# Performance work log

Hardware: AMD Instinct MI355X
Metric: run time of the kernel (lower is better)

Reference implementation:

```python
import jax, jax.numpy as jnp
import numpy as np

B, T, H, C, R = 8, 8192, 128, 128, 128  # batch, points, hidden, c_dim, plane reso
EPS = 1e-3  # 10e-4 in original
PLANE_COLS = ((0, 2), (0, 1), (1, 2))  # xz, xy, yz


def _normalize_coordinate(p, cols):
    # normalize_coordinate with padding=0.0: p in [-0.5,0.5] -> [0,1), clipped
    xy = p[..., jnp.array(cols)] / (1.0 + 0.0 + EPS) + 0.5
    return jnp.clip(xy, 0.0, 1.0 - EPS)


def _coordinate2index(xy):
    g = jnp.floor(xy * R).astype(jnp.int32)  # [B,T,2]
    return g[..., 0] + R * g[..., 1]  # [B,T]


def _resblock(x, w0, b0, w1, b1, ws):
    # ResnetBlockFC: fc_1(relu(fc_0(relu(x)))) + shortcut(x)
    net = jax.nn.relu(x) @ w0 + b0
    dx = jax.nn.relu(net) @ w1 + b1
    return x @ ws + dx


def _pool_local(c, idx_list):
    # c: [B,T,F]; scatter_max into R*R bins per plane, gather back, sum over planes
    def one(cb, ib):  # cb [T,F], ib [T]
        out = jnp.full((R * R, cb.shape[-1]), -jnp.inf, cb.dtype).at[ib].max(cb)
        out = jnp.where(jnp.isinf(out), jnp.zeros_like(out), out)  # empty bins -> 0
        return out[ib]  # gather-broadcast back to points
    pooled = jnp.zeros_like(c)
    for idx in idx_list:
        pooled = pooled + jax.vmap(one)(c, idx)
    return pooled


def _plane_features(cfeat, idx):
    # scatter_mean of [B,T,C] into [B, C, R, R]
    def one(cb, ib):  # cb [T,C], ib [T]
        sums = jnp.zeros((R * R, cb.shape[-1]), cb.dtype).at[ib].add(cb)
        cnt = jnp.zeros((R * R,), cb.dtype).at[ib].add(1.0)
        return sums / jnp.clip(cnt, 1.0, None)[:, None]
    m = jax.vmap(one)(cfeat, idx)  # [B, R*R, C]
    return m.transpose(0, 2, 1).reshape(cfeat.shape[0], cfeat.shape[-1], R, R)


def _forward(p, p2, wp, bp, wp2, bp2,
             blk_w0, blk_b0, blk_w1, blk_b1, blk_ws,
             blkc_w0, blkc_b0, blkc_w1, blkc_b1, blkc_ws,
             fc_c_w, fc_c_b, fc_cc_w, fc_cc_b):
    idx_list = [_coordinate2index(_normalize_coordinate(p, cols)) for cols in PLANE_COLS]

    # feat_pos (PointNetPlusPlusAttnFusion) surrogate: per-point projections + additive fusion
    net = p @ wp + bp                  # [B,T,2H] geometry stream
    net_corr = net + (p2 @ wp2 + bp2)  # [B,T,2H] fused articulation stream

    net = _resblock(net, blk_w0[0], blk_b0[0], blk_w1[0], blk_b1[0], blk_ws[0])
    for i in range(1, blk_w0.shape[0]):
        pooled = _pool_local(net, idx_list)
        net = _resblock(jnp.concatenate([net, pooled], axis=-1),
                        blk_w0[i], blk_b0[i], blk_w1[i], blk_b1[i], blk_ws[i])
    c = net @ fc_c_w + fc_c_b  # [B,T,C]

    net_corr = _resblock(net_corr, blkc_w0[0], blkc_b0[0], blkc_w1[0], blkc_b1[0], blkc_ws[0])
    for i in range(1, blkc_w0.shape[0]):
        pooled = _pool_local(net_corr, idx_list)
        net_corr = _resblock(jnp.concatenate([net_corr, pooled], axis=-1),
                             blkc_w0[i], blkc_b0[i], blkc_w1[i], blkc_b1[i], blkc_ws[i])
    c_corr = net_corr @ fc_cc_w + fc_cc_b  # [B,T,C]

    planes = [_plane_features(c, idx) for idx in idx_list]
    planes += [_plane_features(c_corr, idx) for idx in idx_list]
    # order: geo_xz, geo_xy, geo_yz, corr_xz, corr_xy, corr_yz
    return jnp.stack(planes)  # [6, B, C, R, R]


def setup_inputs() -> dict:
    key = jax.random.key(0)
    ks = jax.random.split(key, 24)
    s = 0.05
    def n(i, shape):
        return jax.random.normal(ks[i], shape, jnp.float32) * s
    NB = 5
    return {
        "p": jax.random.uniform(ks[0], (B, T, 3), jnp.float32, -0.5, 0.5),
        "p2": jax.random.uniform(ks[1], (B, T, 3), jnp.float32, -0.5, 0.5),
        "wp": n(2, (3, 2 * H)), "bp": jnp.zeros((2 * H,), jnp.float32),
        "wp2": n(3, (3, 2 * H)), "bp2": jnp.zeros((2 * H,), jnp.float32),
        "blk_w0": n(4, (NB, 2 * H, H)), "blk_b0": jnp.zeros((NB, H), jnp.float32),
        "blk_w1": n(5, (NB, H, H)), "blk_b1": jnp.zeros((NB, H), jnp.float32),
        "blk_ws": n(6, (NB, 2 * H, H)),
        "blkc_w0": n(7, (NB, 2 * H, H)), "blkc_b0": jnp.zeros((NB, H), jnp.float32),
        "blkc_w1": n(8, (NB, H, H)), "blkc_b1": jnp.zeros((NB, H), jnp.float32),
        "blkc_ws": n(9, (NB, 2 * H, H)),
        "fc_c_w": n(10, (H, C)), "fc_c_b": jnp.zeros((C,), jnp.float32),
        "fc_cc_w": n(11, (H, C)), "fc_cc_b": jnp.zeros((C,), jnp.float32),
    }


def reference(p, p2, wp, bp, wp2, bp2,
              blk_w0, blk_b0, blk_w1, blk_b1, blk_ws,
              blkc_w0, blkc_b0, blkc_w1, blkc_b1, blkc_ws,
              fc_c_w, fc_c_b, fc_cc_w, fc_cc_b):
    return _forward(p, p2, wp, bp, wp2, bp2,
                    blk_w0, blk_b0, blk_w1, blk_b1, blk_ws,
                    blkc_w0, blkc_b0, blkc_w1, blkc_b1, blkc_ws,
                    fc_c_w, fc_c_b, fc_cc_w, fc_cc_b)
```

## Files before the change

kernel.cpp:

```cpp
#include <hip/hip_runtime.h>
#include <cstdint>
#include <cstddef>

#define Bn 8
#define Tn 8192
#define BT (Bn*Tn)
#define Hn 128
#define RRn 16384

typedef unsigned short u16;
typedef __attribute__((ext_vector_type(8))) short s8v;
typedef __attribute__((ext_vector_type(4))) float f4v;

#define SSTR ((size_t)BT*128)

__device__ __forceinline__ u16 f2bf(float f) {
  unsigned u = __float_as_uint(f);
  unsigned r = (u + 0x7FFF + ((u >> 16) & 1)) >> 16;
  return (u16)r;
}
__device__ __forceinline__ unsigned pack2(float a, float b) {
  return (unsigned)f2bf(a) | ((unsigned)f2bf(b) << 16);
}

__device__ __forceinline__ s8v relu8(s8v a) {
  union { s8v s; unsigned u[4]; } x; x.s = a;
#pragma unroll
  for (int k = 0; k < 4; ++k) {
    unsigned m = ((x.u[k] & 0x80008000u) >> 15) * 0xFFFFu;
    x.u[k] &= ~m;
  }
  return x.s;
}

__device__ __forceinline__ void upk(unsigned u, float& lo, float& hi) {
  lo = __uint_as_float(u << 16);
  hi = __uint_as_float(u & 0xFFFF0000u);
}

__global__ void k_idx(const float* __restrict__ p, int* __restrict__ idx) {
  int i = blockIdx.x*256 + threadIdx.x;
  if (i >= BT) return;
  float v0 = p[i*3+0], v1 = p[i*3+1], v2 = p[i*3+2];
  float v[3] = {v0, v1, v2};
  const int A0[3] = {0,0,1};
  const int A1[3] = {2,1,2};
#pragma unroll
  for (int pl = 0; pl < 3; ++pl) {
    float a = v[A0[pl]] / 1.001f + 0.5f;
    float b = v[A1[pl]] / 1.001f + 0.5f;
    a = fminf(fmaxf(a, 0.0f), 0.999f);
    b = fminf(fmaxf(b, 0.0f), 0.999f);
    int ga = (int)floorf(a * 128.0f);
    int gb = (int)floorf(b * 128.0f);
    idx[pl*BT + i] = ga + 128*gb;
  }
}

__global__ void k_hist(const int* __restrict__ idx, int* __restrict__ cnt32) {
  int g = blockIdx.x*256 + threadIdx.x;
  if (g >= 3*BT) return;
  int pl = g >> 16, i = g & (BT-1);
  int b = i >> 13;
  atomicAdd(&cnt32[(pl*Bn + b)*RRn + idx[g]], 1);
}

__global__ void k_scan(const int* __restrict__ cnt32, int* __restrict__ starts,
                       int* __restrict__ cursor) {
  int seg = blockIdx.x;
  const int* c = cnt32 + seg*RRn;
  int* st = starts + seg*RRn;
  int* cu = cursor + seg*RRn;
  int t = threadIdx.x;
  __shared__ int part[256];
  int base = t*64;
  int sum = 0;
#pragma unroll 8
  for (int j = 0; j < 64; ++j) sum += c[base+j];
  part[t] = sum; __syncthreads();
  for (int ofs = 1; ofs < 256; ofs <<= 1) {
    int v = (t >= ofs) ? part[t-ofs] : 0;
    __syncthreads();
    part[t] += v;
    __syncthreads();
  }
  int run = (t ? part[t-1] : 0) + seg*Tn;
#pragma unroll 8
  for (int j = 0; j < 64; ++j) { st[base+j] = run; cu[base+j] = run; run += c[base+j]; }
}

__global__ void k_fill(const int* __restrict__ idx, int* __restrict__ cursor,
                       int* __restrict__ sorted) {
  int g = blockIdx.x*256 + threadIdx.x;
  if (g >= 3*BT) return;
  int pl = g >> 16, i = g & (BT-1);
  int b = i >> 13;
  int pos = atomicAdd(&cursor[(pl*Bn + b)*RRn + idx[g]], 1);
  sorted[pos] = i;
}

__global__ void k_prep(const float* __restrict__ bw0, const float* __restrict__ bw1,
                       const float* __restrict__ bws, const float* __restrict__ cw0,
                       const float* __restrict__ cw1, const float* __restrict__ cws,
                       const float* __restrict__ fcw, const float* __restrict__ fccw,
                       u16* __restrict__ arena) {
  int c = blockIdx.x;
  int s = c / 26, r = c % 26;
  const float* base;
  if (r < 10)      base = (s ? cw0 : bw0) + (size_t)(r >> 1)*32768 + (size_t)(r & 1)*16384;
  else if (r < 15) base = (s ? cw1 : bw1) + (size_t)(r - 10)*16384;
  else if (r < 25) base = (s ? cws : bws) + (size_t)((r - 15) >> 1)*32768 + (size_t)((r - 15) & 1)*16384;
  else             base = s ? fccw : fcw;
  __shared__ u16 ld[128*130];
#pragma unroll 4
  for (int it = 0; it < 64; ++it) {
    int lin = it*256 + threadIdx.x;
    int k = lin >> 7, n = lin & 127;
    ld[k*130 + n] = f2bf(base[lin]);
  }
  __syncthreads();
  u16* dst = arena + (size_t)c*16384;
#pragma unroll 4
  for (int it = 0; it < 64; ++it) {
    int lin = it*256 + threadIdx.x;
    int n = lin >> 7, k = lin & 127;
    dst[lin] = ld[k*130 + n];
  }
}

template<int MODE>
__global__ __launch_bounds__(512) void k_rb(
    const u16* __restrict__ xAb, const u16* __restrict__ xBb,
    const float* __restrict__ p, const float* __restrict__ p2,
    const float* __restrict__ wp, const float* __restrict__ bp,
    const float* __restrict__ wp2, const float* __restrict__ bp2,
    const u16* __restrict__ arena,
    int cw00, int cw01, int cws0, int cws1, int cw1c, int cfcw,
    const float* __restrict__ b0g, const float* __restrict__ b0c,
    const float* __restrict__ b1g, const float* __restrict__ b1c,
    const float* __restrict__ fcbg, const float* __restrict__ fcbc,
    u16* __restrict__ outb)
{
  const int y = blockIdx.y;
  const u16* ar = arena + (size_t)y*26*16384;
  const u16* w00 = ar + (size_t)cw00*16384;
  const u16* w01 = ar + (size_t)cw01*16384;
  const u16* ws0 = ar + (size_t)cws0*16384;
  const u16* ws1 = ar + (size_t)cws1*16384;
  const u16* w1c = ar + (size_t)cw1c*16384;
  const u16* fcw = ar + (size_t)cfcw*16384;
  const float* b0 = y ? b0c : b0g;
  const float* b1 = y ? b1c : b1g;
  const float* fcb = y ? fcbc : fcbg;
  const u16* xA = xAb + (size_t)y*SSTR;
  const u16* xB = xBb + (size_t)y*SSTR;
  u16* outp = outb + (size_t)y*SSTR;

  __shared__ u16 xs [128*72];
  __shared__ u16 w0s[128*72];
  __shared__ u16 wss[128*72];
  __shared__ u16 hid[128*136];
  const int tid = threadIdx.x;
  const size_t row0 = (size_t)blockIdx.x * 128;
  const int l = tid & 63, w = tid >> 6;
  const int lm = l & 15, lg = l >> 4;
  const int trow = tid >> 2, tq = tid & 3;

  f4v acc_h[8], acc_s[8];
#pragma unroll
  for (int j = 0; j < 8; ++j) { acc_h[j] = (f4v){0,0,0,0}; acc_s[j] = (f4v){0,0,0,0}; }

  float pa0=0.f, pa1=0.f, pa2=0.f, pq0=0.f, pq1=0.f, pq2=0.f;
  if (MODE == 1) {
    int rr = (int)row0 + trow;
    pa0 = p[rr*3+0]; pa1 = p[rr*3+1]; pa2 = p[rr*3+2];
    if (y) { pq0 = p2[rr*3+0]; pq1 = p2[rr*3+1]; pq2 = p2[rr*3+2]; }
  }

  const u16* pa  = xs  + (w*16 + lm)*72 + lg*8;
  const u16* pbh = w0s + lm*72 + lg*8;
  const u16* pbs = wss + lm*72 + lg*8;

#pragma unroll 1
  for (int kc = 0; kc < 4; ++kc) {
    const u16* xsrc  = (kc < 2) ? xA  : xB;
    const u16* w0src = (kc < 2) ? w00 : w01;
    const u16* wssrc = (kc < 2) ? ws0 : ws1;
    const int k0 = (kc & 1) * 64;
    __syncthreads();
    {
      if (MODE == 1) {
        const int c0 = (kc >> 1)*128 + k0 + tq*16;
        unsigned tmp[8];
#pragma unroll
        for (int q = 0; q < 4; ++q) {
          float4 w0v = *(const float4*)(wp + c0 + q*4);
          float4 w1v = *(const float4*)(wp + 256 + c0 + q*4);
          float4 w2v = *(const float4*)(wp + 512 + c0 + q*4);
          float4 bbv = *(const float4*)(bp + c0 + q*4);
          float v0 = pa0*w0v.x + pa1*w1v.x + pa2*w2v.x + bbv.x;
          float v1 = pa0*w0v.y + pa1*w1v.y + pa2*w2v.y + bbv.y;
          float v2 = pa0*w0v.z + pa1*w1v.z + pa2*w2v.z + bbv.z;
          float v3 = pa0*w0v.w + pa1*w1v.w + pa2*w2v.w + bbv.w;
          if (y) {
            float4 u0 = *(const float4*)(wp2 + c0 + q*4);
            float4 u1 = *(const float4*)(wp2 + 256 + c0 + q*4);
            float4 u2 = *(const float4*)(wp2 + 512 + c0 + q*4);
            float4 b2 = *(const float4*)(bp2 + c0 + q*4);
            v0 += pq0*u0.x + pq1*u1.x + pq2*u2.x + b2.x;
            v1 += pq0*u0.y + pq1*u1.y + pq2*u2.y + b2.y;
            v2 += pq0*u0.z + pq1*u1.z + pq2*u2.z + b2.z;
            v3 += pq0*u0.w + pq1*u1.w + pq2*u2.w + b2.w;
          }
          tmp[q*2]   = pack2(v0, v1);
          tmp[q*2+1] = pack2(v2, v3);
        }
        uint4* d1 = (uint4*)(xs + trow*72 + tq*16);
        d1[0] = make_uint4(tmp[0], tmp[1], tmp[2], tmp[3]);
        d1[1] = make_uint4(tmp[4], tmp[5], tmp[6], tmp[7]);
      } else {
        const u16* s1 = xsrc + (row0 + trow)*128 + k0 + tq*16;
        uint4* d1 = (uint4*)(xs + trow*72 + tq*16);
        d1[0] = ((const uint4*)s1)[0]; d1[1] = ((const uint4*)s1)[1];
      }
      const u16* s2 = w0src + trow*128 + k0 + tq*16;
      uint4* d2 = (uint4*)(w0s + trow*72 + tq*16);
      d2[0] = ((const uint4*)s2)[0]; d2[1] = ((const uint4*)s2)[1];
      const u16* s3 = wssrc + trow*128 + k0 + tq*16;
      uint4* d3 = (uint4*)(wss + trow*72 + tq*16);
      d3[0] = ((const uint4*)s3)[0]; d3[1] = ((const uint4*)s3)[1];
    }
    __syncthreads();
#pragma unroll
    for (int kk = 0; kk < 2; ++kk) {
      s8v a  = *(const s8v*)(pa + kk*32);
      s8v ar2 = relu8(a);
#pragma unroll
      for (int nj = 0; nj < 8; ++nj) {
        s8v bh = *(const s8v*)(pbh + nj*16*72 + kk*32);
        acc_h[nj] = __builtin_amdgcn_mfma_f32_16x16x32_bf16(ar2, bh, acc_h[nj], 0, 0, 0);
      }
#pragma unroll
      for (int nj = 0; nj < 8; ++nj) {
        s8v bs = *(const s8v*)(pbs + nj*16*72 + kk*32);
        acc_s[nj] = __builtin_amdgcn_mfma_f32_16x16x32_bf16(a, bs, acc_s[nj], 0, 0, 0);
      }
    }
  }
  __syncthreads();
  {
    const u16* s1 = w1c + trow*128 + tq*16;
    uint4* d1 = (uint4*)(w0s + trow*72 + tq*16);
    d1[0] = ((const uint4*)s1)[0]; d1[1] = ((const uint4*)s1)[1];
    const u16* s2 = w1c + trow*128 + 64 + tq*16;
    uint4* d2 = (uint4*)(wss + trow*72 + tq*16);
    d2[0] = ((const uint4*)s2)[0]; d2[1] = ((const uint4*)s2)[1];
#pragma unroll
    for (int nj = 0; nj < 8; ++nj) {
      const int col = nj*16 + lm;
      const float bv = b0[col];
#pragma unroll
      for (int r = 0; r < 4; ++r) {
        int row = w*16 + lg*4 + r;
        hid[row*136 + col] = f2bf(fmaxf(acc_h[nj][r] + bv, 0.0f));
      }
    }
  }
  __syncthreads();
  {
    const u16* pah = hid + (w*16 + lm)*136 + lg*8;
#pragma unroll
    for (int kk = 0; kk < 4; ++kk) {
      s8v a = *(const s8v*)(pah + kk*32);
      const u16* pb = ((kk < 2) ? w0s : wss) + lm*72 + lg*8 + (kk & 1)*32;
#pragma unroll
      for (int nj = 0; nj < 8; ++nj) {
        s8v bb = *(const s8v*)(pb + nj*16*72);
        acc_s[nj] = __builtin_amdgcn_mfma_f32_16x16x32_bf16(a, bb, acc_s[nj], 0, 0, 0);
      }
    }
  }
  if (MODE != 2) {
#pragma unroll
    for (int nj = 0; nj < 8; ++nj) {
      const int col = nj*16 + lm;
      const float bv = b1[col];
#pragma unroll
      for (int r = 0; r < 4; ++r) {
        int row = w*16 + lg*4 + r;
        outp[(row0 + row)*128 + col] = f2bf(acc_s[nj][r] + bv);
      }
    }
  } else {
    __syncthreads();
#pragma unroll
    for (int nj = 0; nj < 8; ++nj) {
      const int col = nj*16 + lm;
      const float bv = b1[col];
#pragma unroll
      for (int r = 0; r < 4; ++r) {
        int row = w*16 + lg*4 + r;
        hid[row*136 + col] = f2bf(acc_s[nj][r] + bv);
      }
    }
    const u16* s1 = fcw + trow*128 + tq*16;
    uint4* d1 = (uint4*)(w0s + trow*72 + tq*16);
    d1[0] = ((const uint4*)s1)[0]; d1[1] = ((const uint4*)s1)[1];
    const u16* s2 = fcw + trow*128 + 64 + tq*16;
    uint4* d2 = (uint4*)(wss + trow*72 + tq*16);
    d2[0] = ((const uint4*)s2)[0]; d2[1] = ((const uint4*)s2)[1];
    __syncthreads();
    f4v accf[8];
#pragma unroll
    for (int j = 0; j < 8; ++j) accf[j] = (f4v){0,0,0,0};
    const u16* pah = hid + (w*16 + lm)*136 + lg*8;
#pragma unroll
    for (int kk = 0; kk < 4; ++kk) {
      s8v a = *(const s8v*)(pah + kk*32);
      const u16* pb = ((kk < 2) ? w0s : wss) + lm*72 + lg*8 + (kk & 1)*32;
#pragma unroll
      for (int nj = 0; nj < 8; ++nj) {
        s8v bb = *(const s8v*)(pb + nj*16*72);
        accf[nj] = __builtin_amdgcn_mfma_f32_16x16x32_bf16(a, bb, accf[nj], 0, 0, 0);
      }
    }
#pragma unroll
    for (int nj = 0; nj < 8; ++nj) {
      const int col = nj*16 + lm;
      const float bv = fcb[col];
#pragma unroll
      for (int r = 0; r < 4; ++r) {
        int row = w*16 + lg*4 + r;
        outp[(row0 + row)*128 + col] = f2bf(accf[nj][r] + bv);
      }
    }
  }
}

__global__ void k_pool(const int* __restrict__ idx, const int* __restrict__ starts,
                       const int* __restrict__ cnt32, const int* __restrict__ sorted,
                       const u16* __restrict__ netb, u16* __restrict__ pooledb) {
  const u16* net = netb + (size_t)blockIdx.y*SSTR;
  u16* pooled = pooledb + (size_t)blockIdx.y*SSTR;
  int g = blockIdx.x*256 + threadIdx.x;
  int sl = g & 15;
  int i = g >> 4;
  if (i >= BT) return;
  int b = i >> 13;
  float acc[8];
#pragma unroll
  for (int k = 0; k < 8; ++k) acc[k] = 0.0f;
#pragma unroll
  for (int pl = 0; pl < 3; ++pl) {
    int seg = (pl*Bn + b)*RRn + idx[pl*BT + i];
    int s = starts[seg];
    int e = s + cnt32[seg];
    float mx[8];
#pragma unroll
    for (int k = 0; k < 8; ++k) mx[k] = -3.0e38f;
    for (int j = s; j < e; ++j) {
      int jj = sorted[j];
      uint4 v = *(const uint4*)(net + (size_t)jj*128 + sl*8);
      float lo, hi;
      upk(v.x, lo, hi); mx[0] = fmaxf(mx[0], lo); mx[1] = fmaxf(mx[1], hi);
      upk(v.y, lo, hi); mx[2] = fmaxf(mx[2], lo); mx[3] = fmaxf(mx[3], hi);
      upk(v.z, lo, hi); mx[4] = fmaxf(mx[4], lo); mx[5] = fmaxf(mx[5], hi);
      upk(v.w, lo, hi); mx[6] = fmaxf(mx[6], lo); mx[7] = fmaxf(mx[7], hi);
    }
#pragma unroll
    for (int k = 0; k < 8; ++k) acc[k] += mx[k];
  }
  union { uint4 v; unsigned u[4]; } o;
#pragma unroll
  for (int k = 0; k < 4; ++k)
    o.u[k] = (unsigned)f2bf(acc[2*k]) | ((unsigned)f2bf(acc[2*k+1]) << 16);
  *(uint4*)(pooled + (size_t)i*128 + sl*8) = o.v;
}

__global__ __launch_bounds__(256) void k_mean(
    const int* __restrict__ starts, const int* __restrict__ cnt32,
    const int* __restrict__ sorted, const u16* __restrict__ cbufb,
    float* __restrict__ out) {
  int W = blockIdx.x*4 + (threadIdx.x >> 6);
  int lane = threadIdx.x & 63;
  int grp = W & 255;
  int b = (W >> 8) & 7;
  int plq = W >> 11;
  int ss = plq / 3, pl = plq - 3*ss;
  int bin = grp*64 + lane;
  int seg = (pl*Bn + b)*RRn + bin;
  int c = cnt32[seg];
  int s0 = starts[seg];
  float inv = (c > 0) ? 1.0f/(float)c : 0.0f;
  const u16* cb = cbufb + (size_t)ss*SSTR;
  size_t obase = ((size_t)(plq*Bn + b)*Hn)*RRn + bin;
#pragma unroll 1
  for (int half = 0; half < 2; ++half) {
    float sum[64];
#pragma unroll
    for (int k = 0; k < 64; ++k) sum[k] = 0.f;
    for (int j = 0; j < c; ++j) {
      int jj = sorted[s0 + j];
      const uint4* r = (const uint4*)(cb + (size_t)jj*128 + half*64);
#pragma unroll
      for (int k = 0; k < 8; ++k) {
        uint4 q = r[k];
        float lo, hi;
        upk(q.x, lo, hi); sum[k*8+0] += lo; sum[k*8+1] += hi;
        upk(q.y, lo, hi); sum[k*8+2] += lo; sum[k*8+3] += hi;
        upk(q.z, lo, hi); sum[k*8+4] += lo; sum[k*8+5] += hi;
        upk(q.w, lo, hi); sum[k*8+6] += lo; sum[k*8+7] += hi;
      }
    }
#pragma unroll
    for (int k = 0; k < 64; ++k)
      out[obase + (size_t)(half*64 + k)*RRn] = sum[k]*inv;
  }
}

extern "C" void kernel_launch(void* const* d_in, const int* in_sizes, int n_in,
                              void* d_out_v, int out_size, void* d_ws, size_t ws_size,
                              hipStream_t stream) {
  const float* p    = (const float*)d_in[0];
  const float* p2   = (const float*)d_in[1];
  const float* wp   = (const float*)d_in[2];
  const float* bp   = (const float*)d_in[3];
  const float* wp2  = (const float*)d_in[4];
  const float* bp2  = (const float*)d_in[5];
  const float* bw0  = (const float*)d_in[6];
  const float* bb0  = (const float*)d_in[7];
  const float* bw1  = (const float*)d_in[8];
  const float* bb1  = (const float*)d_in[9];
  const float* bws  = (const float*)d_in[10];
  const float* cw0  = (const float*)d_in[11];
  const float* cb0  = (const float*)d_in[12];
  const float* cw1  = (const float*)d_in[13];
  const float* cb1  = (const float*)d_in[14];
  const float* cws  = (const float*)d_in[15];
  const float* fcw  = (const float*)d_in[16];
  const float* fcb  = (const float*)d_in[17];
  const float* fccw = (const float*)d_in[18];
  const float* fccb = (const float*)d_in[19];
  float* out = (float*)d_out_v;

  size_t off = 0;
  auto alloc = [&](size_t bytes) -> char* {
    char* r = (char*)d_ws + off;
    off += (bytes + 255) & ~(size_t)255;
    return r;
  };
  int* idx    = (int*)alloc((size_t)3*BT*4);
  int* cnt32  = (int*)alloc((size_t)3*Bn*RRn*4);
  int* starts = (int*)alloc((size_t)3*Bn*RRn*4);
  int* cursor = (int*)alloc((size_t)3*Bn*RRn*4);
  int* sorted = (int*)alloc((size_t)3*BT*4);
  u16* arena  = (u16*)alloc((size_t)52*16384*2);
  u16* buf0   = (u16*)alloc(2*SSTR*2);
  u16* buf1   = (u16*)alloc(2*SSTR*2);
  u16* bufP   = (u16*)alloc(2*SSTR*2);
  u16* cbuf   = (u16*)alloc(2*SSTR*2);
  if (off > ws_size) return;

  hipMemsetAsync(cnt32, 0, (size_t)3*Bn*RRn*4, stream);
  k_prep<<<52, 256, 0, stream>>>(bw0, bw1, bws, cw0, cw1, cws, fcw, fccw, arena);
  k_idx <<<BT/256, 256, 0, stream>>>(p, idx);
  k_hist<<<(3*BT)/256, 256, 0, stream>>>(idx, cnt32);
  k_scan<<<24, 256, 0, stream>>>(cnt32, starts, cursor);
  k_fill<<<(3*BT)/256, 256, 0, stream>>>(idx, cursor, sorted);

  k_rb<1><<<dim3(BT/128, 2), 512, 0, stream>>>(
      nullptr, nullptr, p, p2, wp, bp, wp2, bp2,
      arena, 0, 1, 15, 16, 10, 25,
      bb0, cb0, bb1, cb1, nullptr, nullptr, buf1);
  u16* net = buf1; u16* other = buf0;
  for (int blk = 1; blk < 4; ++blk) {
    k_pool<<<dim3((BT*16)/256, 2), 256, 0, stream>>>(idx, starts, cnt32, sorted, net, bufP);
    k_rb<0><<<dim3(BT/128, 2), 512, 0, stream>>>(
        net, bufP, nullptr, nullptr, nullptr, nullptr, nullptr, nullptr,
        arena, 2*blk, 2*blk+1, 15+2*blk, 16+2*blk, 10+blk, 25,
        bb0 + blk*128, cb0 + blk*128, bb1 + blk*128, cb1 + blk*128,
        nullptr, nullptr, other);
    u16* t = net; net = other; other = t;
  }
  k_pool<<<dim3((BT*16)/256, 2), 256, 0, stream>>>(idx, starts, cnt32, sorted, net, bufP);
  k_rb<2><<<dim3(BT/128, 2), 512, 0, stream>>>(
      net, bufP, nullptr, nullptr, nullptr, nullptr, nullptr, nullptr,
      arena, 8, 9, 23, 24, 14, 25,
      bb0 + 4*128, cb0 + 4*128, bb1 + 4*128, cb1 + 4*128, fcb, fccb, cbuf);

  k_mean<<<3072, 256, 0, stream>>>(starts, cnt32, sorted, cbuf, out);
}
```

Before: 609.1 us.

## Fuse local max-pooling into resblock GEMM loads and histogram into index kernel

Removes the separate k_pool kernel. Each k_rb block now computes the scatter-max pooled features for its rows on the fly while staging the second half of the K dimension into shared memory, which avoids writing and re-reading the pooled buffer. Separately, the histogram atomics move into k_idx, which drops one launch. The cost is that the irregular gather loop now sits inside the GEMM kernel's load phase, which may add register pressure and serialize behind the per-bin loops with uneven counts.

```diff
diff --git a/kernel.cpp b/kernel.cpp
--- a/kernel.cpp
+++ b/kernel.cpp
@@ -38,9 +38,11 @@
   hi = __uint_as_float(u & 0xFFFF0000u);
 }
 
-__global__ void k_idx(const float* __restrict__ p, int* __restrict__ idx) {
+__global__ void k_idx(const float* __restrict__ p, int* __restrict__ idx,
+                      int* __restrict__ cnt32) {
   int i = blockIdx.x*256 + threadIdx.x;
   if (i >= BT) return;
+  int b = i >> 13;
   float v0 = p[i*3+0], v1 = p[i*3+1], v2 = p[i*3+2];
   float v[3] = {v0, v1, v2};
   const int A0[3] = {0,0,1};
@@ -48,21 +50,15 @@
 #pragma unroll
   for (int pl = 0; pl < 3; ++pl) {
     float a = v[A0[pl]] / 1.001f + 0.5f;
-    float b = v[A1[pl]] / 1.001f + 0.5f;
+    float bq = v[A1[pl]] / 1.001f + 0.5f;
     a = fminf(fmaxf(a, 0.0f), 0.999f);
-    b = fminf(fmaxf(b, 0.0f), 0.999f);
+    bq = fminf(fmaxf(bq, 0.0f), 0.999f);
     int ga = (int)floorf(a * 128.0f);
-    int gb = (int)floorf(b * 128.0f);
-    idx[pl*BT + i] = ga + 128*gb;
-  }
-}
-
-__global__ void k_hist(const int* __restrict__ idx, int* __restrict__ cnt32) {
-  int g = blockIdx.x*256 + threadIdx.x;
-  if (g >= 3*BT) return;
-  int pl = g >> 16, i = g & (BT-1);
-  int b = i >> 13;
-  atomicAdd(&cnt32[(pl*Bn + b)*RRn + idx[g]], 1);
+    int gb = (int)floorf(bq * 128.0f);
+    int bin = ga + 128*gb;
+    idx[pl*BT + i] = bin;
+    atomicAdd(&cnt32[(pl*Bn + b)*RRn + bin], 1);
+  }
 }
 
 __global__ void k_scan(const int* __restrict__ cnt32, int* __restrict__ starts,
@@ -130,10 +126,12 @@
 
 template<int MODE>
 __global__ __launch_bounds__(512) void k_rb(
-    const u16* __restrict__ xAb, const u16* __restrict__ xBb,
+    const u16* __restrict__ xAb,
     const float* __restrict__ p, const float* __restrict__ p2,
     const float* __restrict__ wp, const float* __restrict__ bp,
     const float* __restrict__ wp2, const float* __restrict__ bp2,
+    const int* __restrict__ idxg, const int* __restrict__ startsg,
+    const int* __restrict__ cnt32g, const int* __restrict__ sortedg,
     const u16* __restrict__ arena,
     int cw00, int cw01, int cws0, int cws1, int cw1c, int cfcw,
     const float* __restrict__ b0g, const float* __restrict__ b0c,
@@ -153,7 +151,6 @@
   const float* b1 = y ? b1c : b1g;
   const float* fcb = y ? fcbc : fcbg;
   const u16* xA = xAb + (size_t)y*SSTR;
-  const u16* xB = xBb + (size_t)y*SSTR;
   u16* outp = outb + (size_t)y*SSTR;
 
   __shared__ u16 xs [128*72];
@@ -176,6 +173,15 @@
     pa0 = p[rr*3+0]; pa1 = p[rr*3+1]; pa2 = p[rr*3+2];
     if (y) { pq0 = p2[rr*3+0]; pq1 = p2[rr*3+1]; pq2 = p2[rr*3+2]; }
   }
+  int pseg0=0, psegc0=0, pseg1=0, psegc1=0, pseg2=0, psegc2=0;
+  if (MODE != 1) {
+    const int gi = (int)row0 + trow;
+    const int bb = gi >> 13;
+    int s_, c_;
+    s_ = (0*Bn + bb)*RRn + idxg[0*BT + gi]; pseg0 = startsg[s_]; psegc0 = cnt32g[s_];
+    c_ = (1*Bn + bb)*RRn + idxg[1*BT + gi]; pseg1 = startsg[c_]; psegc1 = cnt32g[c_];
+    s_ = (2*Bn + bb)*RRn + idxg[2*BT + gi]; pseg2 = startsg[s_]; psegc2 = cnt32g[s_];
+  }
 
   const u16* pa  = xs  + (w*16 + lm)*72 + lg*8;
   const u16* pbh = w0s + lm*72 + lg*8;
@@ -183,7 +189,6 @@
 
 #pragma unroll 1
   for (int kc = 0; kc < 4; ++kc) {
-    const u16* xsrc  = (kc < 2) ? xA  : xB;
     const u16* w0src = (kc < 2) ? w00 : w01;
     const u16* wssrc = (kc < 2) ? ws0 : ws1;
     const int k0 = (kc & 1) * 64;
@@ -218,10 +223,47 @@
         uint4* d1 = (uint4*)(xs + trow*72 + tq*16);
         d1[0] = make_uint4(tmp[0], tmp[1], tmp[2], tmp[3]);
         d1[1] = make_uint4(tmp[4], tmp[5], tmp[6], tmp[7]);
-      } else {
-        const u16* s1 = xsrc + (row0 + trow)*128 + k0 + tq*16;
+      } else if (kc < 2) {
+        const u16* s1 = xA + (row0 + trow)*128 + k0 + tq*16;
         uint4* d1 = (uint4*)(xs + trow*72 + tq*16);
         d1[0] = ((const uint4*)s1)[0]; d1[1] = ((const uint4*)s1)[1];
+      } else {
+        const int ch0 = k0 + tq*16;
+        float acc[16];
+#pragma unroll
+        for (int k = 0; k < 16; ++k) acc[k] = 0.f;
+        int segS[3] = {pseg0, pseg1, pseg2};
+        int segC[3] = {psegc0, psegc1, psegc2};
+#pragma unroll
+        for (int pl = 0; pl < 3; ++pl) {
+          int s0 = segS[pl];
+          int c  = segC[pl];
+          float mx[16];
+#pragma unroll
+          for (int k = 0; k < 16; ++k) mx[k] = -3.0e38f;
+          for (int j = 0; j < c; ++j) {
+            int jj = sortedg[s0 + j];
+            const uint4* r = (const uint4*)(xA + (size_t)jj*128 + ch0);
+            uint4 q0 = r[0], q1 = r[1];
+            float lo, hi;
+            upk(q0.x, lo, hi); mx[0]=fmaxf(mx[0],lo);  mx[1]=fmaxf(mx[1],hi);
+            upk(q0.y, lo, hi); mx[2]=fmaxf(mx[2],lo);  mx[3]=fmaxf(mx[3],hi);
+            upk(q0.z, lo, hi); mx[4]=fmaxf(mx[4],lo);  mx[5]=fmaxf(mx[5],hi);
+            upk(q0.w, lo, hi); mx[6]=fmaxf(mx[6],lo);  mx[7]=fmaxf(mx[7],hi);
+            upk(q1.x, lo, hi); mx[8]=fmaxf(mx[8],lo);  mx[9]=fmaxf(mx[9],hi);
+            upk(q1.y, lo, hi); mx[10]=fmaxf(mx[10],lo); mx[11]=fmaxf(mx[11],hi);
+            upk(q1.z, lo, hi); mx[12]=fmaxf(mx[12],lo); mx[13]=fmaxf(mx[13],hi);
+            upk(q1.w, lo, hi); mx[14]=fmaxf(mx[14],lo); mx[15]=fmaxf(mx[15],hi);
+          }
+#pragma unroll
+          for (int k = 0; k < 16; ++k) acc[k] += mx[k];
+        }
+        unsigned tmp[8];
+#pragma unroll
+        for (int k = 0; k < 8; ++k) tmp[k] = pack2(acc[2*k], acc[2*k+1]);
+        uint4* d1 = (uint4*)(xs + trow*72 + tq*16);
+        d1[0] = make_uint4(tmp[0], tmp[1], tmp[2], tmp[3]);
+        d1[1] = make_uint4(tmp[4], tmp[5], tmp[6], tmp[7]);
       }
       const u16* s2 = w0src + trow*128 + k0 + tq*16;
       uint4* d2 = (uint4*)(w0s + trow*72 + tq*16);
@@ -335,46 +377,6 @@
       }
     }
   }
-}
-
-__global__ void k_pool(const int* __restrict__ idx, const int* __restrict__ starts,
-                       const int* __restrict__ cnt32, const int* __restrict__ sorted,
-                       const u16* __restrict__ netb, u16* __restrict__ pooledb) {
-  const u16* net = netb + (size_t)blockIdx.y*SSTR;
-  u16* pooled = pooledb + (size_t)blockIdx.y*SSTR;
-  int g = blockIdx.x*256 + threadIdx.x;
-  int sl = g & 15;
-  int i = g >> 4;
-  if (i >= BT) return;
-  int b = i >> 13;
-  float acc[8];
-#pragma unroll
-  for (int k = 0; k < 8; ++k) acc[k] = 0.0f;
-#pragma unroll
-  for (int pl = 0; pl < 3; ++pl) {
-    int seg = (pl*Bn + b)*RRn + idx[pl*BT + i];
-    int s = starts[seg];
-    int e = s + cnt32[seg];
-    float mx[8];
-#pragma unroll
-    for (int k = 0; k < 8; ++k) mx[k] = -3.0e38f;
-    for (int j = s; j < e; ++j) {
-      int jj = sorted[j];
-      uint4 v = *(const uint4*)(net + (size_t)jj*128 + sl*8);
-      float lo, hi;
-      upk(v.x, lo, hi); mx[0] = fmaxf(mx[0], lo); mx[1] = fmaxf(mx[1], hi);
-      upk(v.y, lo, hi); mx[2] = fmaxf(mx[2], lo); mx[3] = fmaxf(mx[3], hi);
-      upk(v.z, lo, hi); mx[4] = fmaxf(mx[4], lo); mx[5] = fmaxf(mx[5], hi);
-      upk(v.w, lo, hi); mx[6] = fmaxf(mx[6], lo); mx[7] = fmaxf(mx[7], hi);
-    }
-#pragma unroll
-    for (int k = 0; k < 8; ++k) acc[k] += mx[k];
-  }
-  union { uint4 v; unsigned u[4]; } o;
-#pragma unroll
-  for (int k = 0; k < 4; ++k)
-    o.u[k] = (unsigned)f2bf(acc[2*k]) | ((unsigned)f2bf(acc[2*k+1]) << 16);
-  *(uint4*)(pooled + (size_t)i*128 + sl*8) = o.v;
 }
 
 __global__ __launch_bounds__(256) void k_mean(
@@ -457,34 +459,33 @@
   u16* arena  = (u16*)alloc((size_t)52*16384*2);
   u16* buf0   = (u16*)alloc(2*SSTR*2);
   u16* buf1   = (u16*)alloc(2*SSTR*2);
-  u16* bufP   = (u16*)alloc(2*SSTR*2);
   u16* cbuf   = (u16*)alloc(2*SSTR*2);
   if (off > ws_size) return;
 
   hipMemsetAsync(cnt32, 0, (size_t)3*Bn*RRn*4, stream);
   k_prep<<<52, 256, 0, stream>>>(bw0, bw1, bws, cw0, cw1, cws, fcw, fccw, arena);
-  k_idx <<<BT/256, 256, 0, stream>>>(p, idx);
-  k_hist<<<(3*BT)/256, 256, 0, stream>>>(idx, cnt32);
+  k_idx <<<BT/256, 256, 0, stream>>>(p, idx, cnt32);
   k_scan<<<24, 256, 0, stream>>>(cnt32, starts, cursor);
   k_fill<<<(3*BT)/256, 256, 0, stream>>>(idx, cursor, sorted);
 
   k_rb<1><<<dim3(BT/128, 2), 512, 0, stream>>>(
-      nullptr, nullptr, p, p2, wp, bp, wp2, bp2,
+      nullptr, p, p2, wp, bp, wp2, bp2,
+      nullptr, nullptr, nullptr, nullptr,
       arena, 0, 1, 15, 16, 10, 25,
       bb0, cb0, bb1, cb1, nullptr, nullptr, buf1);
   u16* net = buf1; u16* other = buf0;
   for (int blk = 1; blk < 4; ++blk) {
-    k_pool<<<dim3((BT*16)/256, 2), 256, 0, stream>>>(idx, starts, cnt32, sorted, net, bufP);
     k_rb<0><<<dim3(BT/128, 2), 512, 0, stream>>>(
-        net, bufP, nullptr, nullptr, nullptr, nullptr, nullptr, nullptr,
+        net, nullptr, nullptr, nullptr, nullptr, nullptr, nullptr,
+        idx, starts, cnt32, sorted,
         arena, 2*blk, 2*blk+1, 15+2*blk, 16+2*blk, 10+blk, 25,
         bb0 + blk*128, cb0 + blk*128, bb1 + blk*128, cb1 + blk*128,
         nullptr, nullptr, other);
     u16* t = net; net = other; other = t;
   }
-  k_pool<<<dim3((BT*16)/256, 2), 256, 0, stream>>>(idx, starts, cnt32, sorted, net, bufP);
   k_rb<2><<<dim3(BT/128, 2), 512, 0, stream>>>(
-      net, bufP, nullptr, nullptr, nullptr, nullptr, nullptr, nullptr,
+      net, nullptr, nullptr, nullptr, nullptr, nullptr, nullptr,
+      idx, starts, cnt32, sorted,
       arena, 8, 9, 23, 24, 14, 25,
       bb0 + 4*128, cb0 + 4*128, bb1 + 4*128, cb1 + 4*128, fcb, fccb, cbuf);
 
```

Result: slower. 657.0 us (+7.9%).

## Double rows per k_rb block, prefetch next K-chunk into registers, fuse histogram into k_idx

Applied to the files above, without the earlier changes.

The resblock GEMM kernel now handles 256 rows per block instead of 128. Each wave computes two 16-row MFMA tiles that share every weight fragment read from LDS. The next K-chunk of activations and weights is loaded into registers while the current chunk's MFMAs run, so global latency overlaps compute. The histogram atomics move into the index kernel, which removes one launch and one pass over idx. The cost is roughly double the accumulator registers and more LDS per block, plus half as many blocks (256 per y), which could hurt occupancy or SM fill.

```diff
diff --git a/kernel.cpp b/kernel.cpp
--- a/kernel.cpp
+++ b/kernel.cpp
@@ -38,9 +38,11 @@
   hi = __uint_as_float(u & 0xFFFF0000u);
 }
 
-__global__ void k_idx(const float* __restrict__ p, int* __restrict__ idx) {
+__global__ void k_idx(const float* __restrict__ p, int* __restrict__ idx,
+                      int* __restrict__ cnt32) {
   int i = blockIdx.x*256 + threadIdx.x;
   if (i >= BT) return;
+  int b = i >> 13;
   float v0 = p[i*3+0], v1 = p[i*3+1], v2 = p[i*3+2];
   float v[3] = {v0, v1, v2};
   const int A0[3] = {0,0,1};
@@ -48,21 +50,15 @@
 #pragma unroll
   for (int pl = 0; pl < 3; ++pl) {
     float a = v[A0[pl]] / 1.001f + 0.5f;
-    float b = v[A1[pl]] / 1.001f + 0.5f;
+    float bq = v[A1[pl]] / 1.001f + 0.5f;
     a = fminf(fmaxf(a, 0.0f), 0.999f);
-    b = fminf(fmaxf(b, 0.0f), 0.999f);
+    bq = fminf(fmaxf(bq, 0.0f), 0.999f);
     int ga = (int)floorf(a * 128.0f);
-    int gb = (int)floorf(b * 128.0f);
-    idx[pl*BT + i] = ga + 128*gb;
-  }
-}
-
-__global__ void k_hist(const int* __restrict__ idx, int* __restrict__ cnt32) {
-  int g = blockIdx.x*256 + threadIdx.x;
-  if (g >= 3*BT) return;
-  int pl = g >> 16, i = g & (BT-1);
-  int b = i >> 13;
-  atomicAdd(&cnt32[(pl*Bn + b)*RRn + idx[g]], 1);
+    int gb = (int)floorf(bq * 128.0f);
+    int bin = ga + 128*gb;
+    idx[pl*BT + i] = bin;
+    atomicAdd(&cnt32[(pl*Bn + b)*RRn + bin], 1);
+  }
 }
 
 __global__ void k_scan(const int* __restrict__ cnt32, int* __restrict__ starts,
@@ -129,7 +125,7 @@
 }
 
 template<int MODE>
-__global__ __launch_bounds__(512) void k_rb(
+__global__ __launch_bounds__(512, 2) void k_rb(
     const u16* __restrict__ xAb, const u16* __restrict__ xBb,
     const float* __restrict__ p, const float* __restrict__ p2,
     const float* __restrict__ wp, const float* __restrict__ bp,
@@ -156,19 +152,22 @@
   const u16* xB = xBb + (size_t)y*SSTR;
   u16* outp = outb + (size_t)y*SSTR;
 
-  __shared__ u16 xs [128*72];
+  __shared__ u16 xs [256*72];
   __shared__ u16 w0s[128*72];
   __shared__ u16 wss[128*72];
-  __shared__ u16 hid[128*136];
+  __shared__ u16 hid[256*136];
   const int tid = threadIdx.x;
-  const size_t row0 = (size_t)blockIdx.x * 128;
+  const size_t row0 = (size_t)blockIdx.x * 256;
   const int l = tid & 63, w = tid >> 6;
   const int lm = l & 15, lg = l >> 4;
-  const int trow = tid >> 2, tq = tid & 3;
-
-  f4v acc_h[8], acc_s[8];
-#pragma unroll
-  for (int j = 0; j < 8; ++j) { acc_h[j] = (f4v){0,0,0,0}; acc_s[j] = (f4v){0,0,0,0}; }
+  const int trow = tid >> 1, th = tid & 1;
+  const int wn = tid >> 2, wq = tid & 3;
+
+  f4v acc_h[2][8], acc_s[2][8];
+#pragma unroll
+  for (int mi = 0; mi < 2; ++mi)
+#pragma unroll
+    for (int j = 0; j < 8; ++j) { acc_h[mi][j] = (f4v){0,0,0,0}; acc_s[mi][j] = (f4v){0,0,0,0}; }
 
   float pa0=0.f, pa1=0.f, pa2=0.f, pq0=0.f, pq1=0.f, pq2=0.f;
   if (MODE == 1) {
@@ -177,163 +176,197 @@
     if (y) { pq0 = p2[rr*3+0]; pq1 = p2[rr*3+1]; pq2 = p2[rr*3+2]; }
   }
 
-  const u16* pa  = xs  + (w*16 + lm)*72 + lg*8;
-  const u16* pbh = w0s + lm*72 + lg*8;
-  const u16* pbs = wss + lm*72 + lg*8;
+  uint4 px0, px1, px2, px3, pwa, pwb, psa, psb;
+  if (MODE != 1) {
+    const uint4* s = (const uint4*)(xA + (row0 + trow)*128 + th*32);
+    px0 = s[0]; px1 = s[1]; px2 = s[2]; px3 = s[3];
+  }
+  {
+    const uint4* sw = (const uint4*)(w00 + wn*128 + wq*16);
+    pwa = sw[0]; pwb = sw[1];
+    const uint4* ss = (const uint4*)(ws0 + wn*128 + wq*16);
+    psa = ss[0]; psb = ss[1];
+  }
 
 #pragma unroll 1
   for (int kc = 0; kc < 4; ++kc) {
-    const u16* xsrc  = (kc < 2) ? xA  : xB;
-    const u16* w0src = (kc < 2) ? w00 : w01;
-    const u16* wssrc = (kc < 2) ? ws0 : ws1;
-    const int k0 = (kc & 1) * 64;
+    if (MODE == 1) {
+      const int c0 = kc*64 + th*32;
+      unsigned t16[16];
+#pragma unroll
+      for (int q = 0; q < 8; ++q) {
+        int c = c0 + q*4;
+        float4 w0v = *(const float4*)(wp + c);
+        float4 w1v = *(const float4*)(wp + 256 + c);
+        float4 w2v = *(const float4*)(wp + 512 + c);
+        float4 bbv = *(const float4*)(bp + c);
+        float v0 = pa0*w0v.x + pa1*w1v.x + pa2*w2v.x + bbv.x;
+        float v1 = pa0*w0v.y + pa1*w1v.y + pa2*w2v.y + bbv.y;
+        float v2 = pa0*w0v.z + pa1*w1v.z + pa2*w2v.z + bbv.z;
+        float v3 = pa0*w0v.w + pa1*w1v.w + pa2*w2v.w + bbv.w;
+        if (y) {
+          float4 u0 = *(const float4*)(wp2 + c);
+          float4 u1 = *(const float4*)(wp2 + 256 + c);
+          float4 u2 = *(const float4*)(wp2 + 512 + c);
+          float4 b2 = *(const float4*)(bp2 + c);
+          v0 += pq0*u0.x + pq1*u1.x + pq2*u2.x + b2.x;
+          v1 += pq0*u0.y + pq1*u1.y + pq2*u2.y + b2.y;
+          v2 += pq0*u0.z + pq1*u1.z + pq2*u2.z + b2.z;
+          v3 += pq0*u0.w + pq1*u1.w + pq2*u2.w + b2.w;
+        }
+        t16[q*2]   = pack2(v0, v1);
+        t16[q*2+1] = pack2(v2, v3);
+      }
+      uint4* d = (uint4*)(xs + trow*72 + th*32);
+      d[0] = make_uint4(t16[0], t16[1], t16[2], t16[3]);
+      d[1] = make_uint4(t16[4], t16[5], t16[6], t16[7]);
+      d[2] = make_uint4(t16[8], t16[9], t16[10], t16[11]);
+      d[3] = make_uint4(t16[12], t16[13], t16[14], t16[15]);
+    } else {
+      uint4* d = (uint4*)(xs + trow*72 + th*32);
+      d[0] = px0; d[1] = px1; d[2] = px2; d[3] = px3;
+    }
+    { uint4* d = (uint4*)(w0s + wn*72 + wq*16); d[0] = pwa; d[1] = pwb; }
+    { uint4* d = (uint4*)(wss + wn*72 + wq*16); d[0] = psa; d[1] = psb; }
+    __syncthreads();
+    if (kc < 3) {
+      const int kn = kc + 1;
+      const int k0n = (kn & 1) * 64;
+      if (MODE != 1) {
+        const u16* xsrcn = (kn < 2) ? xA : xB;
+        const uint4* s = (const uint4*)(xsrcn + (row0 + trow)*128 + k0n + th*32);
+        px0 = s[0]; px1 = s[1]; px2 = s[2]; px3 = s[3];
+      }
+      const u16* w0srcn = (kn < 2) ? w00 : w01;
+      const u16* wssrcn = (kn < 2) ? ws0 : ws1;
+      const uint4* sw = (const uint4*)(w0srcn + wn*128 + k0n + wq*16);
+      pwa = sw[0]; pwb = sw[1];
+      const uint4* ss = (const uint4*)(wssrcn + wn*128 + k0n + wq*16);
+      psa = ss[0]; psb = ss[1];
+    }
+#pragma unroll
+    for (int kk = 0; kk < 2; ++kk) {
+      const int ko = lg*8 + kk*32;
+      s8v a0 = *(const s8v*)(xs + (w*32 + lm)*72 + ko);
+      s8v a1 = *(const s8v*)(xs + (w*32 + 16 + lm)*72 + ko);
+      s8v a0r = relu8(a0), a1r = relu8(a1);
+#pragma unroll
+      for (int nj = 0; nj < 8; ++nj) {
+        s8v bh = *(const s8v*)(w0s + (nj*16 + lm)*72 + ko);
+        acc_h[0][nj] = __builtin_amdgcn_mfma_f32_16x16x32_bf16(a0r, bh, acc_h[0][nj], 0, 0, 0);
+        acc_h[1][nj] = __builtin_amdgcn_mfma_f32_16x16x32_bf16(a1r, bh, acc_h[1][nj], 0, 0, 0);
+      }
+#pragma unroll
+      for (int nj = 0; nj < 8; ++nj) {
+        s8v bs = *(const s8v*)(wss + (nj*16 + lm)*72 + ko);
+        acc_s[0][nj] = __builtin_amdgcn_mfma_f32_16x16x32_bf16(a0, bs, acc_s[0][nj], 0, 0, 0);
+        acc_s[1][nj] = __builtin_amdgcn_mfma_f32_16x16x32_bf16(a1, bs, acc_s[1][nj], 0, 0, 0);
+      }
+    }
+    __syncthreads();
+  }
+  {
+    const uint4* s1 = (const uint4*)(w1c + wn*128 + wq*16);
+    uint4 aa = s1[0], bb2 = s1[1];
+    const uint4* s2 = (const uint4*)(w1c + wn*128 + 64 + wq*16);
+    uint4 cc = s2[0], dd = s2[1];
+    { uint4* d = (uint4*)(w0s + wn*72 + wq*16); d[0] = aa; d[1] = bb2; }
+    { uint4* d = (uint4*)(wss + wn*72 + wq*16); d[0] = cc; d[1] = dd; }
+#pragma unroll
+    for (int mi = 0; mi < 2; ++mi)
+#pragma unroll
+      for (int nj = 0; nj < 8; ++nj) {
+        const int col = nj*16 + lm;
+        const float bv = b0[col];
+#pragma unroll
+        for (int r = 0; r < 4; ++r) {
+          int row = w*32 + mi*16 + lg*4 + r;
+          hid[row*136 + col] = f2bf(fmaxf(acc_h[mi][nj][r] + bv, 0.0f));
+        }
+      }
+  }
+  __syncthreads();
+#pragma unroll
+  for (int kk = 0; kk < 4; ++kk) {
+    const int koA = lg*8 + kk*32;
+    const int koB = lg*8 + (kk & 1)*32;
+    const u16* pb = (kk < 2) ? w0s : wss;
+    s8v a0 = *(const s8v*)(hid + (w*32 + lm)*136 + koA);
+    s8v a1 = *(const s8v*)(hid + (w*32 + 16 + lm)*136 + koA);
+#pragma unroll
+    for (int nj = 0; nj < 8; ++nj) {
+      s8v bb = *(const s8v*)(pb + (nj*16 + lm)*72 + koB);
+      acc_s[0][nj] = __builtin_amdgcn_mfma_f32_16x16x32_bf16(a0, bb, acc_s[0][nj], 0, 0, 0);
+      acc_s[1][nj] = __builtin_amdgcn_mfma_f32_16x16x32_bf16(a1, bb, acc_s[1][nj], 0, 0, 0);
+    }
+  }
+  if (MODE != 2) {
+#pragma unroll
+    for (int mi = 0; mi < 2; ++mi)
+#pragma unroll
+      for (int nj = 0; nj < 8; ++nj) {
+        const int col = nj*16 + lm;
+        const float bv = b1[col];
+#pragma unroll
+        for (int r = 0; r < 4; ++r) {
+          int row = w*32 + mi*16 + lg*4 + r;
+          outp[(row0 + row)*128 + col] = f2bf(acc_s[mi][nj][r] + bv);
+        }
+      }
+  } else {
     __syncthreads();
     {
-      if (MODE == 1) {
-        const int c0 = (kc >> 1)*128 + k0 + tq*16;
-        unsigned tmp[8];
-#pragma unroll
-        for (int q = 0; q < 4; ++q) {
-          float4 w0v = *(const float4*)(wp + c0 + q*4);
-          float4 w1v = *(const float4*)(wp + 256 + c0 + q*4);
-          float4 w2v = *(const float4*)(wp + 512 + c0 + q*4);
-          float4 bbv = *(const float4*)(bp + c0 + q*4);
-          float v0 = pa0*w0v.x + pa1*w1v.x + pa2*w2v.x + bbv.x;
-          float v1 = pa0*w0v.y + pa1*w1v.y + pa2*w2v.y + bbv.y;
-          float v2 = pa0*w0v.z + pa1*w1v.z + pa2*w2v.z + bbv.z;
-          float v3 = pa0*w0v.w + pa1*w1v.w + pa2*w2v.w + bbv.w;
-          if (y) {
-            float4 u0 = *(const float4*)(wp2 + c0 + q*4);
-            float4 u1 = *(const float4*)(wp2 + 256 + c0 + q*4);
-            float4 u2 = *(const float4*)(wp2 + 512 + c0 + q*4);
-            float4 b2 = *(const float4*)(bp2 + c0 + q*4);
-            v0 += pq0*u0.x + pq1*u1.x + pq2*u2.x + b2.x;
-            v1 += pq0*u0.y + pq1*u1.y + pq2*u2.y + b2.y;
-            v2 += pq0*u0.z + pq1*u1.z + pq2*u2.z + b2.z;
-            v3 += pq0*u0.w + pq1*u1.w + pq2*u2.w + b2.w;
+      const uint4* s1 = (const uint4*)(fcw + wn*128 + wq*16);
+      uint4 aa = s1[0], bb2 = s1[1];
+      const uint4* s2 = (const uint4*)(fcw + wn*128 + 64 + wq*16);
+      uint4 cc = s2[0], dd = s2[1];
+      { uint4* d = (uint4*)(w0s + wn*72 + wq*16); d[0] = aa; d[1] = bb2; }
+      { uint4* d = (uint4*)(wss + wn*72 + wq*16); d[0] = cc; d[1] = dd; }
+#pragma unroll
+      for (int mi = 0; mi < 2; ++mi)
+#pragma unroll
+        for (int nj = 0; nj < 8; ++nj) {
+          const int col = nj*16 + lm;
+          const float bv = b1[col];
+#pragma unroll
+          for (int r = 0; r < 4; ++r) {
+            int row = w*32 + mi*16 + lg*4 + r;
+            hid[row*136 + col] = f2bf(acc_s[mi][nj][r] + bv);
           }
-          tmp[q*2]   = pack2(v0, v1);
-          tmp[q*2+1] = pack2(v2, v3);
         }
-        uint4* d1 = (uint4*)(xs + trow*72 + tq*16);
-        d1[0] = make_uint4(tmp[0], tmp[1], tmp[2], tmp[3]);
-        d1[1] = make_uint4(tmp[4], tmp[5], tmp[6], tmp[7]);
-      } else {
-        const u16* s1 = xsrc + (row0 + trow)*128 + k0 + tq*16;
-        uint4* d1 = (uint4*)(xs + trow*72 + tq*16);
-        d1[0] = ((const uint4*)s1)[0]; d1[1] = ((const uint4*)s1)[1];
-      }
-      const u16* s2 = w0src + trow*128 + k0 + tq*16;
-      uint4* d2 = (uint4*)(w0s + trow*72 + tq*16);
-      d2[0] = ((const uint4*)s2)[0]; d2[1] = ((const uint4*)s2)[1];
-      const u16* s3 = wssrc + trow*128 + k0 + tq*16;
-      uint4* d3 = (uint4*)(wss + trow*72 + tq*16);
-      d3[0] = ((const uint4*)s3)[0]; d3[1] = ((const uint4*)s3)[1];
     }
     __syncthreads();
-#pragma unroll
-    for (int kk = 0; kk < 2; ++kk) {
-      s8v a  = *(const s8v*)(pa + kk*32);
-      s8v ar2 = relu8(a);
+    f4v accf[2][8];
+#pragma unroll
+    for (int mi = 0; mi < 2; ++mi)
+#pragma unroll
+      for (int j = 0; j < 8; ++j) accf[mi][j] = (f4v){0,0,0,0};
+#pragma unroll
+    for (int kk = 0; kk < 4; ++kk) {
+      const int koA = lg*8 + kk*32;
+      const int koB = lg*8 + (kk & 1)*32;
+      const u16* pb = (kk < 2) ? w0s : wss;
+      s8v a0 = *(const s8v*)(hid + (w*32 + lm)*136 + koA);
+      s8v a1 = *(const s8v*)(hid + (w*32 + 16 + lm)*136 + koA);
 #pragma unroll
       for (int nj = 0; nj < 8; ++nj) {
-        s8v bh = *(const s8v*)(pbh + nj*16*72 + kk*32);
-        acc_h[nj] = __builtin_amdgcn_mfma_f32_16x16x32_bf16(ar2, bh, acc_h[nj], 0, 0, 0);
-      }
+        s8v bb = *(const s8v*)(pb + (nj*16 + lm)*72 + koB);
+        accf[0][nj] = __builtin_amdgcn_mfma_f32_16x16x32_bf16(a0, bb, accf[0][nj], 0, 0, 0);
+        accf[1][nj] = __builtin_amdgcn_mfma_f32_16x16x32_bf16(a1, bb, accf[1][nj], 0, 0, 0);
+      }
+    }
+#pragma unroll
+    for (int mi = 0; mi < 2; ++mi)
 #pragma unroll
       for (int nj = 0; nj < 8; ++nj) {
-        s8v bs = *(const s8v*)(pbs + nj*16*72 + kk*32);
-        acc_s[nj] = __builtin_amdgcn_mfma_f32_16x16x32_bf16(a, bs, acc_s[nj], 0, 0, 0);
-      }
-    }
-  }
-  __syncthreads();
-  {
-    const u16* s1 = w1c + trow*128 + tq*16;
-    uint4* d1 = (uint4*)(w0s + trow*72 + tq*16);
-    d1[0] = ((const uint4*)s1)[0]; d1[1] = ((const uint4*)s1)[1];
-    const u16* s2 = w1c + trow*128 + 64 + tq*16;
-    uint4* d2 = (uint4*)(wss + trow*72 + tq*16);
-    d2[0] = ((const uint4*)s2)[0]; d2[1] = ((const uint4*)s2)[1];
-#pragma unroll
-    for (int nj = 0; nj < 8; ++nj) {
-      const int col = nj*16 + lm;
-      const float bv = b0[col];
-#pragma unroll
-      for (int r = 0; r < 4; ++r) {
-        int row = w*16 + lg*4 + r;
-        hid[row*136 + col] = f2bf(fmaxf(acc_h[nj][r] + bv, 0.0f));
-      }
-    }
-  }
-  __syncthreads();
-  {
-    const u16* pah = hid + (w*16 + lm)*136 + lg*8;
-#pragma unroll
-    for (int kk = 0; kk < 4; ++kk) {
-      s8v a = *(const s8v*)(pah + kk*32);
-      const u16* pb = ((kk < 2) ? w0s : wss) + lm*72 + lg*8 + (kk & 1)*32;
-#pragma unroll
-      for (int nj = 0; nj < 8; ++nj) {
-        s8v bb = *(const s8v*)(pb + nj*16*72);
-        acc_s[nj] = __builtin_amdgcn_mfma_f32_16x16x32_bf16(a, bb, acc_s[nj], 0, 0, 0);
-      }
-    }
-  }
-  if (MODE != 2) {
-#pragma unroll
-    for (int nj = 0; nj < 8; ++nj) {
-      const int col = nj*16 + lm;
-      const float bv = b1[col];
-#pragma unroll
-      for (int r = 0; r < 4; ++r) {
-        int row = w*16 + lg*4 + r;
-        outp[(row0 + row)*128 + col] = f2bf(acc_s[nj][r] + bv);
-      }
-    }
-  } else {
-    __syncthreads();
-#pragma unroll
-    for (int nj = 0; nj < 8; ++nj) {
-      const int col = nj*16 + lm;
-      const float bv = b1[col];
-#pragma unroll
-      for (int r = 0; r < 4; ++r) {
-        int row = w*16 + lg*4 + r;
-        hid[row*136 + col] = f2bf(acc_s[nj][r] + bv);
-      }
-    }
-    const u16* s1 = fcw + trow*128 + tq*16;
-    uint4* d1 = (uint4*)(w0s + trow*72 + tq*16);
-    d1[0] = ((const uint4*)s1)[0]; d1[1] = ((const uint4*)s1)[1];
-    const u16* s2 = fcw + trow*128 + 64 + tq*16;
-    uint4* d2 = (uint4*)(wss + trow*72 + tq*16);
-    d2[0] = ((const uint4*)s2)[0]; d2[1] = ((const uint4*)s2)[1];
-    __syncthreads();
-    f4v accf[8];
-#pragma unroll
-    for (int j = 0; j < 8; ++j) accf[j] = (f4v){0,0,0,0};
-    const u16* pah = hid + (w*16 + lm)*136 + lg*8;
-#pragma unroll
-    for (int kk = 0; kk < 4; ++kk) {
-      s8v a = *(const s8v*)(pah + kk*32);
-      const u16* pb = ((kk < 2) ? w0s : wss) + lm*72 + lg*8 + (kk & 1)*32;
-#pragma unroll
-      for (int nj = 0; nj < 8; ++nj) {
-        s8v bb = *(const s8v*)(pb + nj*16*72);
-        accf[nj] = __builtin_amdgcn_mfma_f32_16x16x32_bf16(a, bb, accf[nj], 0, 0, 0);
-      }
-    }
-#pragma unroll
-    for (int nj = 0; nj < 8; ++nj) {
-      const int col = nj*16 + lm;
-      const float bv = fcb[col];
-#pragma unroll
-      for (int r = 0; r < 4; ++r) {
-        int row = w*16 + lg*4 + r;
-        outp[(row0 + row)*128 + col] = f2bf(accf[nj][r] + bv);
-      }
-    }
+        const int col = nj*16 + lm;
+        const float bv = fcb[col];
+#pragma unroll
+        for (int r = 0; r < 4; ++r) {
+          int row = w*32 + mi*16 + lg*4 + r;
+          outp[(row0 + row)*128 + col] = f2bf(accf[mi][nj][r] + bv);
+        }
+      }
   }
 }
 
@@ -463,19 +496,18 @@
 
   hipMemsetAsync(cnt32, 0, (size_t)3*Bn*RRn*4, stream);
   k_prep<<<52, 256, 0, stream>>>(bw0, bw1, bws, cw0, cw1, cws, fcw, fccw, arena);
-  k_idx <<<BT/256, 256, 0, stream>>>(p, idx);
-  k_hist<<<(3*BT)/256, 256, 0, stream>>>(idx, cnt32);
+  k_idx <<<BT/256, 256, 0, stream>>>(p, idx, cnt32);
   k_scan<<<24, 256, 0, stream>>>(cnt32, starts, cursor);
   k_fill<<<(3*BT)/256, 256, 0, stream>>>(idx, cursor, sorted);
 
-  k_rb<1><<<dim3(BT/128, 2), 512, 0, stream>>>(
+  k_rb<1><<<dim3(BT/256, 2), 512, 0, stream>>>(
       nullptr, nullptr, p, p2, wp, bp, wp2, bp2,
       arena, 0, 1, 15, 16, 10, 25,
       bb0, cb0, bb1, cb1, nullptr, nullptr, buf1);
   u16* net = buf1; u16* other = buf0;
   for (int blk = 1; blk < 4; ++blk) {
     k_pool<<<dim3((BT*16)/256, 2), 256, 0, stream>>>(idx, starts, cnt32, sorted, net, bufP);
-    k_rb<0><<<dim3(BT/128, 2), 512, 0, stream>>>(
+    k_rb<0><<<dim3(BT/256, 2), 512, 0, stream>>>(
         net, bufP, nullptr, nullptr, nullptr, nullptr, nullptr, nullptr,
         arena, 2*blk, 2*blk+1, 15+2*blk, 16+2*blk, 10+blk, 25,
         bb0 + blk*128, cb0 + blk*128, bb1 + blk*128, cb1 + blk*128,
@@ -483,7 +515,7 @@
     u16* t = net; net = other; other = t;
   }
   k_pool<<<dim3((BT*16)/256, 2), 256, 0, stream>>>(idx, starts, cnt32, sorted, net, bufP);
-  k_rb<2><<<dim3(BT/128, 2), 512, 0, stream>>>(
+  k_rb<2><<<dim3(BT/256, 2), 512, 0, stream>>>(
       net, bufP, nullptr, nullptr, nullptr, nullptr, nullptr, nullptr,
       arena, 8, 9, 23, 24, 14, 25,
       bb0 + 4*128, cb0 + 4*128, bb1 + 4*128, cb1 + 4*128, fcb, fccb, cbuf);
```

After: 526.3 us. 13.6% less time.
